# Kernel optimization log

Measured on AMD Instinct MI355X. Metric: run time of the kernel, lower is better.

Reference implementation:

```python
import jax, jax.numpy as jnp
import numpy as np

WS, SHIFT = 4, 2
Z, H, W = 16, 32, 32
C, HEADS, MLP = 384, 12, 1536
B = 4
N = WS ** 3                      # tokens per 3D window = 64
NW = (Z // WS) * (H // WS) * (W // WS)  # windows per sample = 256
L = Z * H * W
HEAD_DIM = C // HEADS


def _rel_pos_index():
    # replicates meshgrid_3d (which reverses its args) + index arithmetic
    arrs = (np.arange(WS), np.arange(WS), np.arange(WS))  # already symmetric (cubic)
    grids = []
    for i in range(3):
        slc = [1, 1, 1]; slc[i] = WS
        a = arrs[i].reshape(slc)
        for j in range(3):
            if j != i:
                a = a.repeat(WS, axis=j)
        grids.append(a)
    coords = np.stack(grids).reshape(3, -1)            # [3, N]
    rel = coords[:, :, None] - coords[:, None, :]      # [3, N, N]
    rel = rel.transpose(1, 2, 0)                       # [N, N, 3]
    rel[:, :, 0] += WS - 1
    rel[:, :, 1] += WS - 1
    rel[:, :, 2] += WS - 1
    rel[:, :, 0] *= (2 * WS - 1) * (2 * WS - 1)
    rel[:, :, 1] *= 2 * WS - 1
    return rel.sum(-1)                                 # [N, N] ints in [0, (2ws-1)^3)


def _attn_mask():
    # shifted-window mask, exactly as in build()
    m = np.zeros((Z, H, W))
    sl = (slice(0, -WS), slice(-WS, -SHIFT), slice(-SHIFT, None))
    cnt = 0
    for z in sl:
        for h in sl:
            for w in sl:
                m[z, h, w] = cnt
                cnt += 1
    mw = m.reshape(Z // WS, WS, H // WS, WS, W // WS, WS)
    mw = mw.transpose(0, 2, 4, 1, 3, 5).reshape(-1, N)        # [nW, N]
    diff = mw[:, None, :] - mw[:, :, None]                    # [nW, N, N]
    return np.where(diff != 0, -100.0, 0.0).astype(np.float32)


REL_IDX = jnp.asarray(_rel_pos_index())
MASK = jnp.asarray(_attn_mask())


def _ln(x, g, b):
    mu = jnp.mean(x, -1, keepdims=True)
    var = jnp.mean((x - mu) ** 2, -1, keepdims=True)
    return (x - mu) / jnp.sqrt(var + 1e-5) * g + b


def setup_inputs() -> dict:
    key = jax.random.key(0)
    ks = jax.random.split(key, 16)
    s = 0.02
    return {
        "x": jax.random.normal(ks[0], (B, L, C), jnp.float32),
        "norm1_g": jnp.ones((C,), jnp.float32),
        "norm1_b": jnp.zeros((C,), jnp.float32),
        "qkv_w": jax.random.normal(ks[1], (C, 3 * C), jnp.float32) * s,
        "qkv_b": jnp.zeros((3 * C,), jnp.float32),
        "proj_w": jax.random.normal(ks[2], (C, C), jnp.float32) * s,
        "proj_b": jnp.zeros((C,), jnp.float32),
        "rel_bias": jax.random.normal(ks[3], ((2 * WS - 1) ** 3, HEADS), jnp.float32) * s,
        "norm2_g": jnp.ones((C,), jnp.float32),
        "norm2_b": jnp.zeros((C,), jnp.float32),
        "fc1_w": jax.random.normal(ks[4], (C, MLP), jnp.float32) * s,
        "fc1_b": jnp.zeros((MLP,), jnp.float32),
        "fc2_w": jax.random.normal(ks[5], (MLP, C), jnp.float32) * s,
        "fc2_b": jnp.zeros((C,), jnp.float32),
    }


def reference(x, norm1_g, norm1_b, qkv_w, qkv_b, proj_w, proj_b, rel_bias,
              norm2_g, norm2_b, fc1_w, fc1_b, fc2_w, fc2_b):
    b = x.shape[0]
    skip = x
    h = _ln(x, norm1_g, norm1_b).reshape(b, Z, H, W, C)
    h = jnp.roll(h, (-SHIFT, -SHIFT, -SHIFT), axis=(1, 2, 3))
    # window partition -> [b*nW, N, C]
    win = h.reshape(b, Z // WS, WS, H // WS, WS, W // WS, WS, C)
    win = win.transpose(0, 1, 3, 5, 2, 4, 6, 7).reshape(-1, N, C)
    # windowed multi-head attention
    qkv = (win @ qkv_w + qkv_b).reshape(-1, N, 3, HEADS, HEAD_DIM)
    qkv = qkv.transpose(2, 0, 3, 1, 4)                        # [3, bnW, h, N, d]
    q, k, v = qkv[0], qkv[1], qkv[2]
    scale = HEAD_DIM ** -0.5
    attn = jnp.einsum('whnd,whmd->whnm', q * scale, k)        # [bnW, h, N, N]
    bias = rel_bias[REL_IDX.reshape(-1)].reshape(N, N, HEADS).transpose(2, 0, 1)
    attn = attn + bias[None]
    attn = attn.reshape(b, NW, HEADS, N, N) + MASK[None, :, None]
    attn = jax.nn.softmax(attn, axis=-1).reshape(-1, HEADS, N, N)
    o = jnp.einsum('whnm,whmd->whnd', attn, v)
    o = o.transpose(0, 2, 1, 3).reshape(-1, N, C) @ proj_w + proj_b
    # window reverse + unshift
    o = o.reshape(b, Z // WS, H // WS, W // WS, WS, WS, WS, C)
    o = o.transpose(0, 1, 4, 2, 5, 3, 6, 7).reshape(b, Z, H, W, C)
    o = jnp.roll(o, (SHIFT, SHIFT, SHIFT), axis=(1, 2, 3)).reshape(b, L, C)
    x2 = skip + o
    m = _ln(x2, norm2_g, norm2_b)
    m = jax.nn.gelu(m @ fc1_w + fc1_b, approximate=False) @ fc2_w + fc2_b
    return x2 + m
```

## Files before the change

kernel.cpp:

```cpp
#include <hip/hip_runtime.h>
#include <hip/hip_bf16.h>
#include <cstdint>
#include <cmath>


typedef __attribute__((ext_vector_type(4))) float f32x4;
typedef __attribute__((ext_vector_type(8))) __bf16 bf16x8_t;

static __device__ __forceinline__ short f2bf(float f) {
  unsigned u = __builtin_bit_cast(unsigned, f);
  unsigned lsb = (u >> 16) & 1u;
  u += 0x7fffu + lsb;
  return (short)(u >> 16);
}

static __device__ __forceinline__ void gload_lds16(const short* g, short* l) {
  __builtin_amdgcn_global_load_lds(
      (const __attribute__((address_space(1))) void*)g,
      (__attribute__((address_space(3))) void*)l, 16, 0, 0);
}

static constexpr size_t OFF_Q    = 0;
static constexpr size_t OFF_K    = 50331648;
static constexpr size_t OFF_V    = 100663296;
static constexpr size_t OFF_HID  = 0;
static constexpr size_t OFF_WIN  = 201326592;
static constexpr size_t OFF_WQ   = OFF_WIN + 50331648;
static constexpr size_t OFF_WP   = OFF_WQ  + 884736;
static constexpr size_t OFF_W1   = OFF_WP  + 294912;
static constexpr size_t OFF_W2   = OFF_W1  + 1179648;

__global__ void k_w2bf_t(const float* __restrict__ w, short* __restrict__ wt,
                         int K, int N) {
  int idx = blockIdx.x * 256 + threadIdx.x;
  if (idx >= K * N) return;
  int k = idx / N, n = idx - k * N;
  wt[(size_t)n * K + k] = f2bf(w[idx]);
}

__global__ __launch_bounds__(256) void k_ln1_window(
    const float* __restrict__ x, const float* __restrict__ gw,
    const float* __restrict__ gb, short* __restrict__ win) {
  int slot = blockIdx.x * 4 + (threadIdx.x >> 6);
  int lane = threadIdx.x & 63;
  int widx = slot >> 6, n = slot & 63;
  int bidx = widx >> 8, wloc = widx & 255;
  int z = ((wloc >> 6) << 2) + (n >> 4);
  int h = (((wloc >> 3) & 7) << 2) + ((n >> 2) & 3);
  int w = ((wloc & 7) << 2) + (n & 3);
  int zs = (z + 2) & 15, hs = (h + 2) & 31, ws = (w + 2) & 31;
  const float* xp = x + ((size_t)bidx * 16384 + zs * 1024 + hs * 32 + ws) * 384;
  float v[6]; float s = 0.f, s2 = 0.f;
#pragma unroll
  for (int j = 0; j < 6; j++) {
    v[j] = xp[lane + j * 64];
    s += v[j]; s2 += v[j] * v[j];
  }
#pragma unroll
  for (int o = 1; o < 64; o <<= 1) { s += __shfl_xor(s, o); s2 += __shfl_xor(s2, o); }
  float mu = s * (1.f / 384.f);
  float rinv = rsqrtf(s2 * (1.f / 384.f) - mu * mu + 1e-5f);
  short* wp = win + (size_t)slot * 384;
#pragma unroll
  for (int j = 0; j < 6; j++) {
    int c = lane + j * 64;
    wp[c] = f2bf((v[j] - mu) * rinv * gw[c] + gb[c]);
  }
}

__global__ __launch_bounds__(256) void k_ln2(
    const float* __restrict__ x2, const float* __restrict__ gw,
    const float* __restrict__ gb, short* __restrict__ h2) {
  int t = blockIdx.x * 4 + (threadIdx.x >> 6);
  int lane = threadIdx.x & 63;
  const float* xp = x2 + (size_t)t * 384;
  float v[6]; float s = 0.f, s2 = 0.f;
#pragma unroll
  for (int j = 0; j < 6; j++) {
    v[j] = xp[lane + j * 64];
    s += v[j]; s2 += v[j] * v[j];
  }
#pragma unroll
  for (int o = 1; o < 64; o <<= 1) { s += __shfl_xor(s, o); s2 += __shfl_xor(s2, o); }
  float mu = s * (1.f / 384.f);
  float rinv = rsqrtf(s2 * (1.f / 384.f) - mu * mu + 1e-5f);
  short* hp = h2 + (size_t)t * 384;
#pragma unroll
  for (int j = 0; j < 6; j++) {
    int c = lane + j * 64;
    hp[c] = f2bf((v[j] - mu) * rinv * gw[c] + gb[c]);
  }
}

template <int EPI, int KDIM>
__global__ __launch_bounds__(256) void k_gemm(
    const short* __restrict__ A, const short* __restrict__ Bt,
    const float* __restrict__ bias, short* __restrict__ ob0,
    short* __restrict__ ob1, short* __restrict__ ob2,
    const float* __restrict__ aux, float* __restrict__ of32) {
  __shared__ short As[4096];
  __shared__ short Bs[4096];
  const int tid = threadIdx.x;
  const int wave = tid >> 6, lane = tid & 63;
  const int g = lane >> 4, li = lane & 15;
  const int m0 = blockIdx.y << 7, n0 = blockIdx.x << 7;
  const int c0 = wave * 2, c1 = c0 + 1;
  const int row0 = c0 * 16 + (lane >> 2), row1 = c1 * 16 + (lane >> 2);
  const int koff = (lane & 3) * 8;
  const short* gA0 = A + (size_t)(m0 + row0) * KDIM + koff;
  const short* gA1 = A + (size_t)(m0 + row1) * KDIM + koff;
  const short* gB0 = Bt + (size_t)(n0 + row0) * KDIM + koff;
  const short* gB1 = Bt + (size_t)(n0 + row1) * KDIM + koff;
  short* lA0 = As + c0 * 512; short* lA1 = As + c1 * 512;
  short* lB0 = Bs + c0 * 512; short* lB1 = Bs + c1 * 512;
  const int wm = wave >> 1, wn = wave & 1;
  const short* rA = As + (wm * 64 + li) * 32 + g * 8;
  const short* rB = Bs + (wn * 64 + li) * 32 + g * 8;
  f32x4 acc[4][4] = {};
  for (int kt = 0; kt < KDIM; kt += 32) {
    gload_lds16(gA0 + kt, lA0);
    gload_lds16(gA1 + kt, lA1);
    gload_lds16(gB0 + kt, lB0);
    gload_lds16(gB1 + kt, lB1);
    asm volatile("s_waitcnt vmcnt(0)" ::: "memory");
    __syncthreads();
    bf16x8_t a[4], b[4];
#pragma unroll
    for (int i = 0; i < 4; i++) a[i] = *(const bf16x8_t*)(rA + i * 512);
#pragma unroll
    for (int i = 0; i < 4; i++) b[i] = *(const bf16x8_t*)(rB + i * 512);
#pragma unroll
    for (int mi = 0; mi < 4; mi++)
#pragma unroll
      for (int ni = 0; ni < 4; ni++)
        acc[mi][ni] =
            __builtin_amdgcn_mfma_f32_16x16x32_bf16(a[mi], b[ni], acc[mi][ni], 0, 0, 0);
    __syncthreads();
  }
#pragma unroll
  for (int mi = 0; mi < 4; mi++) {
#pragma unroll
    for (int ni = 0; ni < 4; ni++) {
      const int col = n0 + wn * 64 + ni * 16 + li;
      const float bc = bias[col];
      const int rbase = m0 + wm * 64 + mi * 16 + g * 4;
      if constexpr (EPI == 0) {
        const int s = col / 384;
        const int rem = col - s * 384;
        const int head = rem >> 5, d = rem & 31;
#pragma unroll
        for (int r = 0; r < 4; r++) {
          const int row = rbase + r;
          const int widx = row >> 6, n = row & 63;
          float v = acc[mi][ni][r] + bc;
          if (s == 0)
            ob0[(((size_t)widx * 12 + head) * 64 + n) * 32 + d] =
                f2bf(v * 0.17677669529663687f);
          else if (s == 1)
            ob1[(((size_t)widx * 12 + head) * 64 + n) * 32 + d] = f2bf(v);
          else
            ob2[(((size_t)widx * 12 + head) * 32 + d) * 64 + n] = f2bf(v);
        }
      } else if constexpr (EPI == 1) {
#pragma unroll
        for (int r = 0; r < 4; r++) {
          const int row = rbase + r;
          const int widx = row >> 6, n = row & 63;
          const int wloc = widx & 255, bb = widx >> 8;
          const int z = ((wloc >> 6) << 2) + (n >> 4);
          const int h = (((wloc >> 3) & 7) << 2) + ((n >> 2) & 3);
          const int w = ((wloc & 7) << 2) + (n & 3);
          const int zs = (z + 2) & 15, hs = (h + 2) & 31, wsx = (w + 2) & 31;
          const size_t t = (size_t)bb * 16384 + zs * 1024 + hs * 32 + wsx;
          of32[t * 384 + col] = aux[t * 384 + col] + acc[mi][ni][r] + bc;
        }
      } else if constexpr (EPI == 2) {
#pragma unroll
        for (int r = 0; r < 4; r++) {
          const int row = rbase + r;
          float v = acc[mi][ni][r] + bc;
          ob0[(size_t)row * 1536 + col] =
              f2bf(0.5f * v * (1.f + erff(v * 0.70710678118654752f)));
        }
      } else {
#pragma unroll
        for (int r = 0; r < 4; r++) {
          const int row = rbase + r;
          of32[(size_t)row * 384 + col] =
              aux[(size_t)row * 384 + col] + acc[mi][ni][r] + bc;
        }
      }
    }
  }
}

__global__ __launch_bounds__(64) void k_attn(
    const short* __restrict__ qb, const short* __restrict__ kb,
    const short* __restrict__ vb, const float* __restrict__ relb,
    short* __restrict__ owin) {
  __shared__ short pt[64 * 80];
  const int wh_ = blockIdx.x;
  const int widx = wh_ / 12, head = wh_ - widx * 12;
  const int lane = threadIdx.x;
  const int g = lane >> 4, li = lane & 15;
  const short* qp = qb + (size_t)wh_ * 2048;
  const short* kp = kb + (size_t)wh_ * 2048;
  const short* vp = vb + (size_t)wh_ * 2048;
  bf16x8_t kf[4], qf[4];
#pragma unroll
  for (int t = 0; t < 4; t++) {
    kf[t] = *(const bf16x8_t*)(kp + (t * 16 + li) * 32 + g * 8);
    qf[t] = *(const bf16x8_t*)(qp + (t * 16 + li) * 32 + g * 8);
  }
  f32x4 zero = {0.f, 0.f, 0.f, 0.f};
  f32x4 st[4][4];
#pragma unroll
  for (int ti = 0; ti < 4; ti++)
#pragma unroll
    for (int tj = 0; tj < 4; tj++)
      st[ti][tj] = __builtin_amdgcn_mfma_f32_16x16x32_bf16(kf[ti], qf[tj], zero, 0, 0, 0);
  const int wloc = widx & 255;
  const int wz = wloc >> 6, wh2 = (wloc >> 3) & 7, ww2 = wloc & 7;
#pragma unroll
  for (int tj = 0; tj < 4; tj++) {
    const int qn = tj * 16 + li;
    const int qz = qn >> 4, qh = (qn >> 2) & 3, qw = qn & 3;
    const int cq = ((wz < 3) ? 0 : ((qz < 2) ? 1 : 2)) * 9 +
                   ((wh2 < 7) ? 0 : ((qh < 2) ? 1 : 2)) * 3 +
                   ((ww2 < 7) ? 0 : ((qw < 2) ? 1 : 2));
    float mx = -1e30f;
#pragma unroll
    for (int ti = 0; ti < 4; ti++) {
#pragma unroll
      for (int r = 0; r < 4; r++) {
        const int kn = ti * 16 + g * 4 + r;
        const int kz = kn >> 4, kh = (kn >> 2) & 3, kw = kn & 3;
        const int ck = ((wz < 3) ? 0 : ((kz < 2) ? 1 : 2)) * 9 +
                       ((wh2 < 7) ? 0 : ((kh < 2) ? 1 : 2)) * 3 +
                       ((ww2 < 7) ? 0 : ((kw < 2) ? 1 : 2));
        const int idx = (qz - kz + 3) * 49 + (qh - kh + 3) * 7 + (qw - kw + 3);
        float v = st[ti][tj][r] + relb[idx * 12 + head] + ((ck == cq) ? 0.f : -100.f);
        st[ti][tj][r] = v;
        mx = fmaxf(mx, v);
      }
    }
    mx = fmaxf(mx, __shfl_xor(mx, 16));
    mx = fmaxf(mx, __shfl_xor(mx, 32));
    float sum = 0.f;
#pragma unroll
    for (int ti = 0; ti < 4; ti++)
#pragma unroll
      for (int r = 0; r < 4; r++) {
        float e = __expf(st[ti][tj][r] - mx);
        st[ti][tj][r] = e;
        sum += e;
      }
    sum += __shfl_xor(sum, 16);
    sum += __shfl_xor(sum, 32);
    const float rs = 1.f / sum;
#pragma unroll
    for (int ti = 0; ti < 4; ti++)
#pragma unroll
      for (int r = 0; r < 4; r++)
        pt[qn * 80 + ti * 16 + g * 4 + r] = f2bf(st[ti][tj][r] * rs);
  }
  __syncthreads();
  f32x4 o[4][2] = {};
#pragma unroll
  for (int kb2 = 0; kb2 < 2; kb2++) {
    bf16x8_t pa[4], bv[2];
#pragma unroll
    for (int tq = 0; tq < 4; tq++)
      pa[tq] = *(const bf16x8_t*)(pt + (tq * 16 + li) * 80 + kb2 * 32 + g * 8);
#pragma unroll
    for (int td = 0; td < 2; td++)
      bv[td] = *(const bf16x8_t*)(vp + (td * 16 + li) * 64 + kb2 * 32 + g * 8);
#pragma unroll
    for (int tq = 0; tq < 4; tq++)
#pragma unroll
      for (int td = 0; td < 2; td++)
        o[tq][td] = __builtin_amdgcn_mfma_f32_16x16x32_bf16(pa[tq], bv[td], o[tq][td], 0, 0, 0);
  }
#pragma unroll
  for (int tq = 0; tq < 4; tq++)
#pragma unroll
    for (int td = 0; td < 2; td++)
#pragma unroll
      for (int r = 0; r < 4; r++) {
        const int qn = tq * 16 + g * 4 + r;
        const int d = td * 16 + li;
        owin[((size_t)widx * 64 + qn) * 384 + head * 32 + d] = f2bf(o[tq][td][r]);
      }
}

extern "C" void kernel_launch(void* const* d_in, const int* in_sizes, int n_in,
                              void* d_out, int out_size, void* d_ws,
                              size_t ws_size, hipStream_t stream) {
  (void)in_sizes; (void)n_in; (void)out_size; (void)ws_size;
  const float* x      = (const float*)d_in[0];
  const float* n1g    = (const float*)d_in[1];
  const float* n1b    = (const float*)d_in[2];
  const float* qkv_w  = (const float*)d_in[3];
  const float* qkv_b  = (const float*)d_in[4];
  const float* proj_w = (const float*)d_in[5];
  const float* proj_b = (const float*)d_in[6];
  const float* relb   = (const float*)d_in[7];
  const float* n2g    = (const float*)d_in[8];
  const float* n2b    = (const float*)d_in[9];
  const float* fc1_w  = (const float*)d_in[10];
  const float* fc1_b  = (const float*)d_in[11];
  const float* fc2_w  = (const float*)d_in[12];
  const float* fc2_b  = (const float*)d_in[13];
  float* out = (float*)d_out;
  char* ws = (char*)d_ws;

  short* qbuf = (short*)(ws + OFF_Q);
  short* kbuf = (short*)(ws + OFF_K);
  short* vbuf = (short*)(ws + OFF_V);
  short* hid  = (short*)(ws + OFF_HID);
  short* win  = (short*)(ws + OFF_WIN);
  short* owin = (short*)(ws + OFF_WIN);
  short* h2   = (short*)(ws + OFF_WIN);
  float* x2   = out;
  short* wq   = (short*)(ws + OFF_WQ);
  short* wp   = (short*)(ws + OFF_WP);
  short* w1   = (short*)(ws + OFF_W1);
  short* w2   = (short*)(ws + OFF_W2);

  k_w2bf_t<<<(384 * 1152 + 255) / 256, 256, 0, stream>>>(qkv_w, wq, 384, 1152);
  k_w2bf_t<<<(384 * 384 + 255) / 256, 256, 0, stream>>>(proj_w, wp, 384, 384);
  k_w2bf_t<<<(384 * 1536 + 255) / 256, 256, 0, stream>>>(fc1_w, w1, 384, 1536);
  k_w2bf_t<<<(1536 * 384 + 255) / 256, 256, 0, stream>>>(fc2_w, w2, 1536, 384);

  k_ln1_window<<<16384, 256, 0, stream>>>(x, n1g, n1b, win);
  k_gemm<0, 384><<<dim3(9, 512), 256, 0, stream>>>(win, wq, qkv_b, qbuf, kbuf,
                                                   vbuf, nullptr, nullptr);
  k_attn<<<1024 * 12, 64, 0, stream>>>(qbuf, kbuf, vbuf, relb, owin);
  k_gemm<1, 384><<<dim3(3, 512), 256, 0, stream>>>(owin, wp, proj_b, nullptr,
                                                   nullptr, nullptr, x, x2);
  k_ln2<<<16384, 256, 0, stream>>>(x2, n2g, n2b, h2);
  k_gemm<2, 384><<<dim3(12, 512), 256, 0, stream>>>(h2, w1, fc1_b, hid, nullptr,
                                                    nullptr, nullptr, nullptr);
  k_gemm<3, 1536><<<dim3(3, 512), 256, 0, stream>>>(hid, w2, fc2_b, nullptr,
                                                    nullptr, nullptr, x2, out);
}
```

Measured before the change: 793.5 us.

## Double-buffer GEMM with swizzled LDS, XCD block remap, vectorised LN, 4-wave attention

The GEMM now uses a K-tile of 64 with two LDS buffers, so the next tile's global-to-LDS load is issued before the current tile's MFMAs. LDS is XOR-swizzled to avoid bank conflicts, and block IDs are remapped across the 8 XCDs to improve L2 locality. The LayerNorm kernels load float2 and store paired bf16, and attention packs four window-heads per 256-thread block. The trade-off is higher LDS use per GEMM block, which may lower occupancy.

Result: no change. 805.0 us (+1.4%).

```diff
diff --git a/kernel.cpp b/kernel.cpp
--- a/kernel.cpp
+++ b/kernel.cpp
@@ -50,11 +50,11 @@
   int w = ((wloc & 7) << 2) + (n & 3);
   int zs = (z + 2) & 15, hs = (h + 2) & 31, ws = (w + 2) & 31;
   const float* xp = x + ((size_t)bidx * 16384 + zs * 1024 + hs * 32 + ws) * 384;
-  float v[6]; float s = 0.f, s2 = 0.f;
-#pragma unroll
-  for (int j = 0; j < 6; j++) {
-    v[j] = xp[lane + j * 64];
-    s += v[j]; s2 += v[j] * v[j];
+  float2 u[3]; float s = 0.f, s2 = 0.f;
+#pragma unroll
+  for (int j = 0; j < 3; j++) {
+    u[j] = *(const float2*)(xp + lane * 2 + j * 128);
+    s += u[j].x + u[j].y; s2 += u[j].x * u[j].x + u[j].y * u[j].y;
   }
 #pragma unroll
   for (int o = 1; o < 64; o <<= 1) { s += __shfl_xor(s, o); s2 += __shfl_xor(s2, o); }
@@ -62,9 +62,12 @@
   float rinv = rsqrtf(s2 * (1.f / 384.f) - mu * mu + 1e-5f);
   short* wp = win + (size_t)slot * 384;
 #pragma unroll
-  for (int j = 0; j < 6; j++) {
-    int c = lane + j * 64;
-    wp[c] = f2bf((v[j] - mu) * rinv * gw[c] + gb[c]);
+  for (int j = 0; j < 3; j++) {
+    int c = lane * 2 + j * 128;
+    ushort2 o;
+    o.x = (unsigned short)f2bf((u[j].x - mu) * rinv * gw[c] + gb[c]);
+    o.y = (unsigned short)f2bf((u[j].y - mu) * rinv * gw[c + 1] + gb[c + 1]);
+    *(ushort2*)(wp + c) = o;
   }
 }
 
@@ -74,11 +77,11 @@
   int t = blockIdx.x * 4 + (threadIdx.x >> 6);
   int lane = threadIdx.x & 63;
   const float* xp = x2 + (size_t)t * 384;
-  float v[6]; float s = 0.f, s2 = 0.f;
-#pragma unroll
-  for (int j = 0; j < 6; j++) {
-    v[j] = xp[lane + j * 64];
-    s += v[j]; s2 += v[j] * v[j];
+  float2 u[3]; float s = 0.f, s2 = 0.f;
+#pragma unroll
+  for (int j = 0; j < 3; j++) {
+    u[j] = *(const float2*)(xp + lane * 2 + j * 128);
+    s += u[j].x + u[j].y; s2 += u[j].x * u[j].x + u[j].y * u[j].y;
   }
 #pragma unroll
   for (int o = 1; o < 64; o <<= 1) { s += __shfl_xor(s, o); s2 += __shfl_xor(s2, o); }
@@ -86,9 +89,12 @@
   float rinv = rsqrtf(s2 * (1.f / 384.f) - mu * mu + 1e-5f);
   short* hp = h2 + (size_t)t * 384;
 #pragma unroll
-  for (int j = 0; j < 6; j++) {
-    int c = lane + j * 64;
-    hp[c] = f2bf((v[j] - mu) * rinv * gw[c] + gb[c]);
+  for (int j = 0; j < 3; j++) {
+    int c = lane * 2 + j * 128;
+    ushort2 o;
+    o.x = (unsigned short)f2bf((u[j].x - mu) * rinv * gw[c] + gb[c]);
+    o.y = (unsigned short)f2bf((u[j].y - mu) * rinv * gw[c + 1] + gb[c + 1]);
+    *(ushort2*)(hp + c) = o;
   }
 }
 
@@ -98,45 +104,82 @@
     const float* __restrict__ bias, short* __restrict__ ob0,
     short* __restrict__ ob1, short* __restrict__ ob2,
     const float* __restrict__ aux, float* __restrict__ of32) {
-  __shared__ short As[4096];
-  __shared__ short Bs[4096];
+  __shared__ short As[16384];
+  __shared__ short Bs[16384];
   const int tid = threadIdx.x;
   const int wave = tid >> 6, lane = tid & 63;
   const int g = lane >> 4, li = lane & 15;
-  const int m0 = blockIdx.y << 7, n0 = blockIdx.x << 7;
-  const int c0 = wave * 2, c1 = c0 + 1;
-  const int row0 = c0 * 16 + (lane >> 2), row1 = c1 * 16 + (lane >> 2);
-  const int koff = (lane & 3) * 8;
-  const short* gA0 = A + (size_t)(m0 + row0) * KDIM + koff;
-  const short* gA1 = A + (size_t)(m0 + row1) * KDIM + koff;
-  const short* gB0 = Bt + (size_t)(n0 + row0) * KDIM + koff;
-  const short* gB1 = Bt + (size_t)(n0 + row1) * KDIM + koff;
-  short* lA0 = As + c0 * 512; short* lA1 = As + c1 * 512;
-  short* lB0 = Bs + c0 * 512; short* lB1 = Bs + c1 * 512;
+
+  const int nx = gridDim.x;
+  const int nwg = nx * gridDim.y;
+  int bid = blockIdx.y * nx + blockIdx.x;
+  const int cpx = nwg >> 3;
+  bid = (bid & 7) * cpx + (bid >> 3);
+  const int m0 = (bid / nx) << 7, n0 = (bid % nx) << 7;
+
+  const int srow = tid >> 3;
+  const int sc8 = (tid & 7) ^ (srow & 7);
+  const short* gA = A + (size_t)(m0 + srow) * KDIM + sc8 * 8;
+  const short* gB = Bt + (size_t)(n0 + srow) * KDIM + sc8 * 8;
+  short* lA = As + wave * 512;
+  short* lB = Bs + wave * 512;
+
   const int wm = wave >> 1, wn = wave & 1;
-  const short* rA = As + (wm * 64 + li) * 32 + g * 8;
-  const short* rB = Bs + (wn * 64 + li) * 32 + g * 8;
+  const int kx = (li & 7) << 3;
+  const short* ra = As + (wm * 64 + li) * 64;
+  const short* rb = Bs + (wn * 64 + li) * 64;
+  const int c00 = (g * 8) ^ kx;
+  const int c32 = (32 + g * 8) ^ kx;
+
   f32x4 acc[4][4] = {};
-  for (int kt = 0; kt < KDIM; kt += 32) {
-    gload_lds16(gA0 + kt, lA0);
-    gload_lds16(gA1 + kt, lA1);
-    gload_lds16(gB0 + kt, lB0);
-    gload_lds16(gB1 + kt, lB1);
+
+#define STAGE(buf, kt)                                                        \
+  do {                                                                        \
+    _Pragma("unroll") for (int p = 0; p < 4; p++) {                           \
+      gload_lds16(gA + (size_t)(p * 32) * KDIM + (kt),                        \
+                  lA + (buf) * 8192 + p * 2048);                              \
+      gload_lds16(gB + (size_t)(p * 32) * KDIM + (kt),                        \
+                  lB + (buf) * 8192 + p * 2048);                              \
+    }                                                                         \
+  } while (0)
+
+#define COMPUTE(buf)                                                          \
+  do {                                                                        \
+    const short* ra_ = ra + (buf) * 8192;                                     \
+    const short* rb_ = rb + (buf) * 8192;                                     \
+    bf16x8_t a0[4], a1[4], b0[4], b1[4];                                      \
+    _Pragma("unroll") for (int i = 0; i < 4; i++) {                           \
+      a0[i] = *(const bf16x8_t*)(ra_ + i * 1024 + c00);                       \
+      a1[i] = *(const bf16x8_t*)(ra_ + i * 1024 + c32);                       \
+      b0[i] = *(const bf16x8_t*)(rb_ + i * 1024 + c00);                       \
+      b1[i] = *(const bf16x8_t*)(rb_ + i * 1024 + c32);                       \
+    }                                                                         \
+    _Pragma("unroll") for (int mi = 0; mi < 4; mi++)                          \
+        _Pragma("unroll") for (int ni = 0; ni < 4; ni++) acc[mi][ni] =        \
+        __builtin_amdgcn_mfma_f32_16x16x32_bf16(a0[mi], b0[ni], acc[mi][ni],  \
+                                                0, 0, 0);                     \
+    _Pragma("unroll") for (int mi = 0; mi < 4; mi++)                          \
+        _Pragma("unroll") for (int ni = 0; ni < 4; ni++) acc[mi][ni] =        \
+        __builtin_amdgcn_mfma_f32_16x16x32_bf16(a1[mi], b1[ni], acc[mi][ni],  \
+                                                0, 0, 0);                     \
+  } while (0)
+
+  constexpr int NT = KDIM / 64;
+  STAGE(0, 0);
+  asm volatile("s_waitcnt vmcnt(0)" ::: "memory");
+  __syncthreads();
+  int cur = 0;
+  for (int t = 0; t < NT - 1; ++t) {
+    STAGE(cur ^ 1, (t + 1) * 64);
+    COMPUTE(cur);
     asm volatile("s_waitcnt vmcnt(0)" ::: "memory");
     __syncthreads();
-    bf16x8_t a[4], b[4];
-#pragma unroll
-    for (int i = 0; i < 4; i++) a[i] = *(const bf16x8_t*)(rA + i * 512);
-#pragma unroll
-    for (int i = 0; i < 4; i++) b[i] = *(const bf16x8_t*)(rB + i * 512);
-#pragma unroll
-    for (int mi = 0; mi < 4; mi++)
-#pragma unroll
-      for (int ni = 0; ni < 4; ni++)
-        acc[mi][ni] =
-            __builtin_amdgcn_mfma_f32_16x16x32_bf16(a[mi], b[ni], acc[mi][ni], 0, 0, 0);
-    __syncthreads();
-  }
+    cur ^= 1;
+  }
+  COMPUTE(cur);
+#undef STAGE
+#undef COMPUTE
+
 #pragma unroll
   for (int mi = 0; mi < 4; mi++) {
 #pragma unroll
@@ -194,18 +237,20 @@
   }
 }
 
-__global__ __launch_bounds__(64) void k_attn(
+__global__ __launch_bounds__(256) void k_attn(
     const short* __restrict__ qb, const short* __restrict__ kb,
     const short* __restrict__ vb, const float* __restrict__ relb,
     short* __restrict__ owin) {
-  __shared__ short pt[64 * 80];
-  const int wh_ = blockIdx.x;
+  __shared__ short pt[4][5120];
+  const int wave = threadIdx.x >> 6;
+  const int wh_ = blockIdx.x * 4 + wave;
   const int widx = wh_ / 12, head = wh_ - widx * 12;
-  const int lane = threadIdx.x;
+  const int lane = threadIdx.x & 63;
   const int g = lane >> 4, li = lane & 15;
   const short* qp = qb + (size_t)wh_ * 2048;
   const short* kp = kb + (size_t)wh_ * 2048;
   const short* vp = vb + (size_t)wh_ * 2048;
+  short* ptw = pt[wave];
   bf16x8_t kf[4], qf[4];
 #pragma unroll
   for (int t = 0; t < 4; t++) {
@@ -262,7 +307,7 @@
     for (int ti = 0; ti < 4; ti++)
 #pragma unroll
       for (int r = 0; r < 4; r++)
-        pt[qn * 80 + ti * 16 + g * 4 + r] = f2bf(st[ti][tj][r] * rs);
+        ptw[qn * 80 + ti * 16 + g * 4 + r] = f2bf(st[ti][tj][r] * rs);
   }
   __syncthreads();
   f32x4 o[4][2] = {};
@@ -271,7 +316,7 @@
     bf16x8_t pa[4], bv[2];
 #pragma unroll
     for (int tq = 0; tq < 4; tq++)
-      pa[tq] = *(const bf16x8_t*)(pt + (tq * 16 + li) * 80 + kb2 * 32 + g * 8);
+      pa[tq] = *(const bf16x8_t*)(ptw + (tq * 16 + li) * 80 + kb2 * 32 + g * 8);
 #pragma unroll
     for (int td = 0; td < 2; td++)
       bv[td] = *(const bf16x8_t*)(vp + (td * 16 + li) * 64 + kb2 * 32 + g * 8);
@@ -335,7 +380,7 @@
   k_ln1_window<<<16384, 256, 0, stream>>>(x, n1g, n1b, win);
   k_gemm<0, 384><<<dim3(9, 512), 256, 0, stream>>>(win, wq, qkv_b, qbuf, kbuf,
                                                    vbuf, nullptr, nullptr);
-  k_attn<<<1024 * 12, 64, 0, stream>>>(qbuf, kbuf, vbuf, relb, owin);
+  k_attn<<<3072, 256, 0, stream>>>(qbuf, kbuf, vbuf, relb, owin);
   k_gemm<1, 384><<<dim3(3, 512), 256, 0, stream>>>(owin, wp, proj_b, nullptr,
                                                    nullptr, nullptr, x, x2);
   k_ln2<<<16384, 256, 0, stream>>>(x2, n2g, n2b, h2);
```
